# Optimization experiments

Measured on AMD Instinct MI355X. Metric: run time of the kernel, lower is better.

## Reference

```python
import jax, jax.numpy as jnp
import numpy as np

N, E = 50000, 500000
A, R, EB, EH, H, C, AH, SH, S, AV = 64, 20, 32, 64, 4, 32, 128, 64, 32, 32
EPS = 1e-8
MAX_DIST = 0.5   # nm, maximum_interaction_radius
SCALE = 1.0      # nm, scale_factor


def physnet_rbf(d):
    # PhysNet radial basis: exp(-beta * (exp(-d) - mu_k)^2), mu_k in [exp(-r_cut), 1]
    mu = jnp.linspace(np.exp(-MAX_DIST), 1.0, R).astype(jnp.float32)
    beta = jnp.float32((2.0 / R * (1.0 - np.exp(-MAX_DIST))) ** -2)
    return jnp.exp(-beta * (jnp.exp(-d)[:, None] - mu) ** 2)  # [E, R]


def _forward(h, x, v, idx_i, idx_j, W_edge_in, b_edge_in, W_edge_h, b_edge_h,
             W_edge_out, b_edge_out, W_att, b_att, W_x_mix, W_node1, b_node1,
             W_node2, b_node2, W_post1, b_post1, W_post2, b_post2,
             W_vel1, b_vel1, W_vel2, w_v_mix):
    n = h.shape[0]
    act = jax.nn.silu
    seg_sum = lambda t, idx: jax.ops.segment_sum(t, idx, num_segments=n)

    # geometry
    r_ij = x[idx_j] - x[idx_i]                       # [E,3]
    d_ij = jnp.sqrt(jnp.sum(r_ij * r_ij, -1) + EPS)  # [E]
    dir_ij = r_ij / (d_ij[:, None] + EPS)            # [E,3]

    # update_edge: gather, RBF filter, edge MLP
    h_cat = jnp.concatenate([h[idx_i], h[idx_j]], -1)                 # [E,2A]
    filtered = physnet_rbf(d_ij) * (h_cat @ W_edge_in + b_edge_in)    # [E,R]
    e_in = jnp.concatenate([h_cat, filtered, d_ij[:, None] / SCALE], -1)
    h_ij_edge = act(e_in @ W_edge_h + b_edge_h) @ W_edge_out + b_edge_out  # [E,EB]

    # semantic attention: CELU logits + segment softmax over receivers per head
    logits = jax.nn.celu(h_ij_edge @ W_att + b_att, alpha=2.0)        # [E,H]
    seg_max = jax.ops.segment_max(logits, idx_i, num_segments=n)      # [n,H]
    exp_l = jnp.exp(logits - seg_max[idx_i])
    denom = seg_sum(exp_l, idx_i)
    att = exp_l / (denom[idx_i] + EPS)                                # [E,H]
    h_ij_semantic = (att[:, :, None] * h_ij_edge[:, None, :]).reshape(-1, H * EB)

    # neighborhood aggregation (scatter-add)
    h_i_semantic = seg_sum(h_ij_semantic, idx_i)                      # [n,H*EB]

    # spatial attention
    mix = jnp.tanh(h_ij_semantic @ W_x_mix)                           # [E,C]
    combinations = dir_ij[:, None, :] * mix[:, :, None]               # [E,C,3]
    counts = jnp.maximum(seg_sum(jnp.ones((idx_i.shape[0],), h.dtype), idx_i), 1.0)
    comb_mean = seg_sum(combinations, idx_i) / counts[:, None, None]  # scatter-mean
    comb_norm2 = jnp.sum(comb_mean * comb_mean, -1)                   # [n,C]
    h_i_spatial = act(act(comb_norm2 @ W_post1 + b_post1) @ W_post2 + b_post2)

    # node update (residual)
    node_in = jnp.concatenate([h, h_i_semantic, h_i_spatial], -1)
    h_upd = h + act(act(node_in @ W_node1 + b_node1) @ W_node2 + b_node2)

    # velocity / coordinate update
    v_ij = jnp.einsum('ecx,c->ex', combinations, w_v_mix)             # [E,3]
    dv = seg_sum(v_ij, idx_i) / counts[:, None]                       # scatter-mean
    gate = 2.0 * jax.nn.sigmoid(act(h_upd @ W_vel1 + b_vel1) @ W_vel2)  # [n,1]
    v_upd = gate * v + dv
    x_upd = x + v_upd
    return h_upd, x_upd, v_upd


def _p(k, shape, scale=0.05):
    return jax.random.normal(k, shape, dtype=jnp.float32) * scale


def setup_inputs() -> dict:
    key = jax.random.key(0)
    ks = jax.random.split(key, 24)
    return {
        'h': jax.random.normal(ks[0], (N, A), dtype=jnp.float32),
        'x': jax.random.normal(ks[1], (N, 3), dtype=jnp.float32),
        'v': jax.random.normal(ks[2], (N, 3), dtype=jnp.float32),
        'idx_i': jax.random.randint(ks[3], (E,), 0, N),
        'idx_j': jax.random.randint(ks[4], (E,), 0, N),
        'W_edge_in': _p(ks[5], (2 * A, R)), 'b_edge_in': jnp.zeros((R,), jnp.float32),
        'W_edge_h': _p(ks[6], (2 * A + R + 1, EH)), 'b_edge_h': jnp.zeros((EH,), jnp.float32),
        'W_edge_out': _p(ks[7], (EH, EB)), 'b_edge_out': jnp.zeros((EB,), jnp.float32),
        'W_att': _p(ks[8], (EB, H)), 'b_att': jnp.zeros((H,), jnp.float32),
        'W_x_mix': _p(ks[9], (H * EB, C)),
        'W_node1': _p(ks[10], (A + H * EB + S, AH)), 'b_node1': jnp.zeros((AH,), jnp.float32),
        'W_node2': _p(ks[11], (AH, A)), 'b_node2': jnp.zeros((A,), jnp.float32),
        'W_post1': _p(ks[12], (C, SH)), 'b_post1': jnp.zeros((SH,), jnp.float32),
        'W_post2': _p(ks[13], (SH, S)), 'b_post2': jnp.zeros((S,), jnp.float32),
        'W_vel1': _p(ks[14], (A, AV)), 'b_vel1': jnp.zeros((AV,), jnp.float32),
        'W_vel2': _p(ks[15], (AV, 1)),
        'w_v_mix': _p(ks[16], (C,)),
    }


def reference(h, x, v, idx_i, idx_j, W_edge_in, b_edge_in, W_edge_h, b_edge_h,
              W_edge_out, b_edge_out, W_att, b_att, W_x_mix, W_node1, b_node1,
              W_node2, b_node2, W_post1, b_post1, W_post2, b_post2,
              W_vel1, b_vel1, W_vel2, w_v_mix):
    return _forward(h, x, v, idx_i, idx_j, W_edge_in, b_edge_in, W_edge_h, b_edge_h,
                    W_edge_out, b_edge_out, W_att, b_att, W_x_mix, W_node1, b_node1,
                    W_node2, b_node2, W_post1, b_post1, W_post2, b_post2,
                    W_vel1, b_vel1, W_vel2, w_v_mix)
```

## Files before the change

### kernel.cpp

```cpp
#include <hip/hip_runtime.h>
#include <math.h>

#define DA 64
#define NODEIN_DIM 224
#define EPSC 1e-8f

typedef short v8s __attribute__((ext_vector_type(8)));
typedef float v4f __attribute__((ext_vector_type(4)));
typedef unsigned short ushort_t;

__device__ __forceinline__ float siluf(float v) { return v / (1.0f + __expf(-v)); }

__device__ __forceinline__ void atomAddF(float* p, float v) {
#if defined(__HIP_DEVICE_COMPILE__)
  unsafeAtomicAdd(p, v);
#else
  atomicAdd(p, v);
#endif
}

__device__ __forceinline__ unsigned short f2bfu(float f) {
  union { float f; unsigned u; } v; v.f = f;
  unsigned r = v.u + 0x7fffu + ((v.u >> 16) & 1u);
  return (unsigned short)(r >> 16);
}
__device__ __forceinline__ short f2bfs(float f) { return (short)f2bfu(f); }
__device__ __forceinline__ float bf2f(ushort_t s) {
  union { unsigned u; float f; } v; v.u = ((unsigned)s) << 16; return v.f;
}

#define MU0 0.60653065971263342f
#define DMU ((1.0f - 0.60653065971263342f) / 19.0f)
#define BETA ((float)(1.0 / (0.039346934028736658 * 0.039346934028736658)))

__global__ __launch_bounds__(256) void cast_h(
    const float* __restrict__ hsrc, ushort_t* __restrict__ hb, int n4)
{
  const int i = blockIdx.x * blockDim.x + threadIdx.x;
  if (i < n4) {
    const float4 fv = ((const float4*)hsrc)[i];
    ushort4 o;
    o.x = f2bfu(fv.x); o.y = f2bfu(fv.y); o.z = f2bfu(fv.z); o.w = f2bfu(fv.w);
    ((ushort4*)hb)[i] = o;
  }
}

__global__ __launch_bounds__(256) void deg_count(
    const int* __restrict__ idx_i, int* __restrict__ deg, int E)
{
  const int stride = gridDim.x * blockDim.x;
  for (int e = blockIdx.x * blockDim.x + threadIdx.x; e < E; e += stride)
    atomicAdd(&deg[idx_i[e]], 1);
}

#define SCAN_B 64
#define SCAN_T (SCAN_B * 256)

__global__ __launch_bounds__(256) void deg_tsum(
    const int* __restrict__ deg, int* __restrict__ tsum, int N, int C)
{
  const int g = blockIdx.x * blockDim.x + threadIdx.x;
  const int lo = g * C;
  const int hi = (lo + C < N) ? (lo + C) : N;
  int s = 0;
  for (int i = lo; i < hi; ++i) s += deg[i];
  tsum[g] = s;
}

__global__ __launch_bounds__(256) void scan_tsum(int* __restrict__ tsum)
{
  __shared__ int ps[256];
  const int t = threadIdx.x;
  const int per = SCAN_T / 256;
  const int lo = t * per;
  int s = 0;
  for (int i = 0; i < per; ++i) s += tsum[lo + i];
  ps[t] = s;
  __syncthreads();
  if (t == 0) {
    int a = 0;
    for (int i = 0; i < 256; ++i) { const int v = ps[i]; ps[i] = a; a += v; }
  }
  __syncthreads();
  int acc = ps[t];
  for (int i = 0; i < per; ++i) {
    const int v = tsum[lo + i];
    tsum[lo + i] = acc;
    acc += v;
  }
}

__global__ __launch_bounds__(256) void write_csr(
    const int* __restrict__ deg, const int* __restrict__ tpre,
    int* __restrict__ rowstart, int* __restrict__ cursor,
    float* __restrict__ counts, int N, int C)
{
  const int g = blockIdx.x * blockDim.x + threadIdx.x;
  const int lo = g * C;
  const int hi = (lo + C < N) ? (lo + C) : N;
  int acc = tpre[g];
  for (int i = lo; i < hi; ++i) {
    const int d = deg[i];
    rowstart[i] = acc;
    cursor[i] = acc;
    counts[i] = (float)d;
    acc += d;
  }
  if (hi == N) rowstart[N] = acc;
}

__global__ __launch_bounds__(256) void bucket_edges(
    const int* __restrict__ idx_i, const int* __restrict__ idx_j,
    int* __restrict__ cursor, int* __restrict__ iperm,
    int* __restrict__ jperm, int E)
{
  const int stride = gridDim.x * blockDim.x;
  for (int e = blockIdx.x * blockDim.x + threadIdx.x; e < E; e += stride) {
    const int ii = idx_i[e];
    const int pos = atomicAdd(&cursor[ii], 1);
    iperm[pos] = ii;
    jperm[pos] = idx_j[e];
  }
}

#define THS 72
__global__ __launch_bounds__(256) void edge_f12(
    const ushort_t* __restrict__ h_bf, const float* __restrict__ x,
    const int* __restrict__ iperm, const int* __restrict__ jperm,
    const float* __restrict__ W_in, const float* __restrict__ b_in,
    const float* __restrict__ W_h, const float* __restrict__ b_h,
    const float* __restrict__ W_out, const float* __restrict__ b_out,
    const float* __restrict__ W_att, const float* __restrict__ b_att,
    float* __restrict__ dirb, ushort_t* __restrict__ heb,
    float* __restrict__ expl, float* __restrict__ denom, int E)
{
  __shared__ ushort_t sB1[8 * 512];
  __shared__ ushort_t sB2[20 * 512];
  __shared__ ushort_t tH[4][16 * THS];

  const int tid = threadIdx.x;
  for (int idx = tid; idx < 8 * 512; idx += 256) {
    const int j = idx & 7;
    const int ln = (idx >> 3) & 63;
    const int f = idx >> 9;
    const int k = (f >> 1) * 32 + (ln >> 4) * 8 + j;
    const int col = (f & 1) * 16 + (ln & 15);
    sB1[idx] = (col < 20) ? f2bfu(W_in[k * 20 + col]) : (ushort_t)0;
  }
  for (int idx = tid; idx < 20 * 512; idx += 256) {
    const int j = idx & 7;
    const int ln = (idx >> 3) & 63;
    const int f = idx >> 9;
    const int k = (f >> 2) * 32 + (ln >> 4) * 8 + j;
    const int col = (f & 3) * 16 + (ln & 15);
    sB2[idx] = (k < 149) ? f2bfu(W_h[k * 64 + col]) : (ushort_t)0;
  }
  __syncthreads();

  const int gtid = blockIdx.x * blockDim.x + tid;
  const int wid = gtid >> 6;
  const int lane = tid & 63;
  const int w = tid >> 6;
  const int nw = (gridDim.x * blockDim.x) >> 6;
  const int l15 = lane & 15;
  const int q = lane >> 4;

  const ushort_t* b1l = sB1 + lane * 8;
  const ushort_t* b2l = sB2 + lane * 8;

  v8s bfr3[2][2];
  #pragma unroll
  for (int kc = 0; kc < 2; ++kc)
    #pragma unroll
    for (int nt = 0; nt < 2; ++nt)
      #pragma unroll
      for (int j = 0; j < 8; ++j) {
        const int k = kc * 32 + q * 8 + j;
        const int col = nt * 16 + l15;
        bfr3[kc][nt][j] = f2bfs(W_out[k * 32 + col]);
      }

  float bin[2], mu[2];
  #pragma unroll
  for (int nt = 0; nt < 2; ++nt) {
    const int col = nt * 16 + l15;
    bin[nt] = (col < 20) ? b_in[col] : 0.0f;
    mu[nt] = MU0 + (float)col * DMU;
  }
  float bias2[4];
  #pragma unroll
  for (int nt = 0; nt < 4; ++nt) bias2[nt] = b_h[nt * 16 + l15];
  float bias3[2];
  #pragma unroll
  for (int nt = 0; nt < 2; ++nt) bias3[nt] = b_out[nt * 16 + l15];

  v8s battf;
  #pragma unroll
  for (int j = 0; j < 8; ++j)
    battf[j] = (l15 < 4) ? f2bfs(W_att[(q * 8 + j) * 4 + l15]) : (short)0;
  const float bav = (l15 < 4) ? b_att[l15] : 0.0f;

  const int ntiles = (E + 15) >> 4;

  int iiC = 0, jjC = 0;
  v8s afr[4];
  if (wid < ntiles) {
    const int row0 = wid * 16 + l15;
    const int rowL0 = (row0 < E) ? row0 : (E - 1);
    iiC = iperm[rowL0];
    jjC = jperm[rowL0];
    afr[0] = *(const v8s*)(h_bf + (size_t)iiC * 64 + q * 8);
    afr[1] = *(const v8s*)(h_bf + (size_t)iiC * 64 + 32 + q * 8);
    afr[2] = *(const v8s*)(h_bf + (size_t)jjC * 64 + q * 8);
    afr[3] = *(const v8s*)(h_bf + (size_t)jjC * 64 + 32 + q * 8);
  }

  for (int t = wid; t < ntiles; t += nw) {
    const int tn = t + nw;
    int iiN = 0, jjN = 0;
    v8s nfr[4];
    if (tn < ntiles) {
      const int rowN = tn * 16 + l15;
      const int rowLN = (rowN < E) ? rowN : (E - 1);
      iiN = iperm[rowLN];
      jjN = jperm[rowLN];
      nfr[0] = *(const v8s*)(h_bf + (size_t)iiN * 64 + q * 8);
      nfr[1] = *(const v8s*)(h_bf + (size_t)iiN * 64 + 32 + q * 8);
      nfr[2] = *(const v8s*)(h_bf + (size_t)jjN * 64 + q * 8);
      nfr[3] = *(const v8s*)(h_bf + (size_t)jjN * 64 + 32 + q * 8);
    }

    const int row = t * 16 + l15;
    float dval = 0.0f;
    if (lane < 16 && row < E) {
      const float rx = x[jjC * 3 + 0] - x[iiC * 3 + 0];
      const float ry = x[jjC * 3 + 1] - x[iiC * 3 + 1];
      const float rz = x[jjC * 3 + 2] - x[iiC * 3 + 2];
      const float d = sqrtf(rx * rx + ry * ry + rz * rz + EPSC);
      dval = d;
      const float inv = 1.0f / (d + EPSC);
      dirb[row * 3 + 0] = rx * inv;
      dirb[row * 3 + 1] = ry * inv;
      dirb[row * 3 + 2] = rz * inv;
    }

    v4f acc1[2];
    #pragma unroll
    for (int nt = 0; nt < 2; ++nt) {
      v4f a = {0.f, 0.f, 0.f, 0.f};
      #pragma unroll
      for (int kc = 0; kc < 4; ++kc) {
        const v8s bfrag = *(const v8s*)(b1l + (kc * 2 + nt) * 512);
        a = __builtin_amdgcn_mfma_f32_16x16x32_bf16(afr[kc], bfrag, a, 0, 0, 0);
      }
      acc1[nt] = a;
    }

    float dr[4], edr[4];
    #pragma unroll
    for (int r = 0; r < 4; ++r) {
      dr[r] = __shfl(dval, q * 4 + r);
      edr[r] = __expf(-dr[r]);
    }
    #pragma unroll
    for (int nt = 0; nt < 2; ++nt) {
      const int col = nt * 16 + l15;
      #pragma unroll
      for (int r = 0; r < 4; ++r) {
        ushort_t ov;
        if (col < 20) {
          const float tt = edr[r] - mu[nt];
          ov = f2bfu((acc1[nt][r] + bin[nt]) * __expf(-BETA * tt * tt));
        } else if (col == 20) {
          ov = f2bfu(dr[r]);
        } else {
          ov = 0;
        }
        tH[w][(q * 4 + r) * THS + col] = ov;
      }
    }
    __builtin_amdgcn_wave_barrier();

    const v8s afr4 = *(const v8s*)&tH[w][l15 * THS + q * 8];
    __builtin_amdgcn_wave_barrier();

    v4f acc2[4];
    #pragma unroll
    for (int nt = 0; nt < 4; ++nt) {
      v4f a = {0.f, 0.f, 0.f, 0.f};
      #pragma unroll
      for (int kc = 0; kc < 4; ++kc) {
        const v8s bfrag = *(const v8s*)(b2l + (kc * 4 + nt) * 512);
        a = __builtin_amdgcn_mfma_f32_16x16x32_bf16(afr[kc], bfrag, a, 0, 0, 0);
      }
      const v8s bfrag4 = *(const v8s*)(b2l + (4 * 4 + nt) * 512);
      a = __builtin_amdgcn_mfma_f32_16x16x32_bf16(afr4, bfrag4, a, 0, 0, 0);
      acc2[nt] = a;
    }

    #pragma unroll
    for (int nt = 0; nt < 4; ++nt) {
      #pragma unroll
      for (int r = 0; r < 4; ++r)
        tH[w][(q * 4 + r) * THS + nt * 16 + l15] =
            f2bfu(siluf(acc2[nt][r] + bias2[nt]));
    }
    __builtin_amdgcn_wave_barrier();

    v8s af3[2];
    af3[0] = *(const v8s*)&tH[w][l15 * THS + q * 8];
    af3[1] = *(const v8s*)&tH[w][l15 * THS + 32 + q * 8];

    v4f acc3[2];
    #pragma unroll
    for (int nt = 0; nt < 2; ++nt) {
      v4f a = {0.f, 0.f, 0.f, 0.f};
      #pragma unroll
      for (int kc = 0; kc < 2; ++kc)
        a = __builtin_amdgcn_mfma_f32_16x16x32_bf16(af3[kc], bfr3[kc][nt], a, 0, 0, 0);
      acc3[nt] = a;
    }
    __builtin_amdgcn_wave_barrier();

    const int rowb = t * 16 + q * 4;
    #pragma unroll
    for (int nt = 0; nt < 2; ++nt) {
      const int col = nt * 16 + l15;
      #pragma unroll
      for (int r = 0; r < 4; ++r) {
        const ushort_t hv = f2bfu(acc3[nt][r] + bias3[nt]);
        tH[w][(q * 4 + r) * THS + col] = hv;
        if (rowb + r < E) heb[(size_t)(rowb + r) * 32 + col] = hv;
      }
    }
    __builtin_amdgcn_wave_barrier();

    const v8s afA = *(const v8s*)&tH[w][l15 * THS + q * 8];
    v4f az = {0.f, 0.f, 0.f, 0.f};
    const v4f aacc = __builtin_amdgcn_mfma_f32_16x16x32_bf16(afA, battf, az, 0, 0, 0);

    int ii_r[4];
    #pragma unroll
    for (int r = 0; r < 4; ++r) ii_r[r] = __shfl(iiC, q * 4 + r);

    if (l15 < 4) {
      #pragma unroll
      for (int r = 0; r < 4; ++r) {
        if (rowb + r < E) {
          const float la = aacc[r] + bav;
          const float l = (la > 0.f) ? la : 2.0f * (__expf(0.5f * la) - 1.0f);
          const float ev = __expf(l);
          expl[(size_t)(rowb + r) * 4 + l15] = ev;
          atomAddF(&denom[ii_r[r] * 4 + l15], ev);
        }
      }
    }
    __builtin_amdgcn_wave_barrier();

    iiC = iiN; jjC = jjN;
    afr[0] = nfr[0]; afr[1] = nfr[1]; afr[2] = nfr[2]; afr[3] = nfr[3];
  }
}

__global__ __launch_bounds__(256) void mix_kernel(
    const ushort_t* __restrict__ heb, const int* __restrict__ iperm,
    const float* __restrict__ expl, const float* __restrict__ denom,
    const float* __restrict__ W_xmix, const float* __restrict__ w_vmix,
    ushort_t* __restrict__ mixE, float* __restrict__ pE, int E)
{
  const int tid = blockIdx.x * blockDim.x + threadIdx.x;
  const int wid = tid >> 6;
  const int lane = threadIdx.x & 63;
  const int nw = (gridDim.x * blockDim.x) >> 6;
  const int l15 = lane & 15;
  const int q = lane >> 4;

  v8s bfr[4][2];
  #pragma unroll
  for (int kc = 0; kc < 4; ++kc)
    #pragma unroll
    for (int nt = 0; nt < 2; ++nt)
      #pragma unroll
      for (int j = 0; j < 8; ++j) {
        const int k = kc * 32 + q * 8 + j;
        const int col = nt * 16 + l15;
        bfr[kc][nt][j] = f2bfs(W_xmix[k * 32 + col]);
      }
  float wv[2];
  wv[0] = w_vmix[l15];
  wv[1] = w_vmix[16 + l15];

  const int ntiles = (E + 15) >> 4;
  for (int t = wid; t < ntiles; t += nw) {
    const int row = t * 16 + l15;
    const int rowL = (row < E) ? row : (E - 1);
    const int ii = iperm[rowL];
    float att[4];
    #pragma unroll
    for (int hh = 0; hh < 4; ++hh)
      att[hh] = expl[(size_t)rowL * 4 + hh] / (denom[ii * 4 + hh] + EPSC);

    const v8s hech = *(const v8s*)(heb + (size_t)rowL * 32 + q * 8);
    float hef[8];
    #pragma unroll
    for (int j = 0; j < 8; ++j) hef[j] = bf2f((ushort_t)hech[j]);

    v8s afr[4];
    #pragma unroll
    for (int kc = 0; kc < 4; ++kc)
      #pragma unroll
      for (int j = 0; j < 8; ++j)
        afr[kc][j] = f2bfs(att[kc] * hef[j]);

    v4f acc[2];
    #pragma unroll
    for (int nt = 0; nt < 2; ++nt) {
      v4f a = {0.f, 0.f, 0.f, 0.f};
      #pragma unroll
      for (int kc = 0; kc < 4; ++kc)
        a = __builtin_amdgcn_mfma_f32_16x16x32_bf16(afr[kc], bfr[kc][nt], a, 0, 0, 0);
      acc[nt] = a;
    }

    const int rowb = t * 16 + q * 4;
    float pr[4];
    #pragma unroll
    for (int r = 0; r < 4; ++r) {
      const float m0 = tanhf(acc[0][r]);
      const float m1 = tanhf(acc[1][r]);
      if (rowb + r < E) {
        mixE[(size_t)(rowb + r) * 32 + l15] = f2bfu(m0);
        mixE[(size_t)(rowb + r) * 32 + 16 + l15] = f2bfu(m1);
      }
      pr[r] = m0 * wv[0] + m1 * wv[1];
    }
    #pragma unroll
    for (int r = 0; r < 4; ++r) {
      pr[r] += __shfl_xor(pr[r], 1);
      pr[r] += __shfl_xor(pr[r], 2);
      pr[r] += __shfl_xor(pr[r], 4);
      pr[r] += __shfl_xor(pr[r], 8);
      if (l15 == 0 && rowb + r < E) pE[rowb + r] = pr[r];
    }
  }
}

__global__ __launch_bounds__(256) void node_reduce(
    const int* __restrict__ rowstart,
    const ushort_t* __restrict__ heb, const ushort_t* __restrict__ mixE,
    const float* __restrict__ expl, const float* __restrict__ denom,
    const float* __restrict__ dirb, const float* __restrict__ pE,
    ushort_t* __restrict__ hsem, float* __restrict__ comb_sum,
    float* __restrict__ dv_sum, int N)
{
  const int tid = blockIdx.x * blockDim.x + threadIdx.x;
  const int wid = tid >> 6;
  const int lane = threadIdx.x & 63;
  const int nw = (gridDim.x * blockDim.x) >> 6;
  const int hh = lane >> 5;
  const int eb = lane & 31;

  for (int n = wid; n < N; n += nw) {
    const int s = rowstart[n];
    const int epd = rowstart[n + 1];
    float semA = 0.f, semB = 0.f;
    float cx = 0.f, cy = 0.f, cz = 0.f;
    float dvx = 0.f, dvy = 0.f, dvz = 0.f;
    int k = s;
    const int e4 = s + ((epd - s) & ~3);
    for (; k < e4; k += 4) {
      float he[4], ea[4], ec[4], dx[4], dy[4], dz[4], m[4], pe[4];
      #pragma unroll
      for (int u = 0; u < 4; ++u) {
        he[u] = bf2f(heb[(size_t)(k + u) * 32 + eb]);
        ea[u] = expl[(size_t)(k + u) * 4 + hh];
        ec[u] = expl[(size_t)(k + u) * 4 + 2 + hh];
        dx[u] = dirb[(k + u) * 3 + 0];
        dy[u] = dirb[(k + u) * 3 + 1];
        dz[u] = dirb[(k + u) * 3 + 2];
      }
      if (lane < 32) {
        #pragma unroll
        for (int u = 0; u < 4; ++u)
          m[u] = bf2f(mixE[(size_t)(k + u) * 32 + lane]);
      }
      if (lane == 0) {
        #pragma unroll
        for (int u = 0; u < 4; ++u) pe[u] = pE[k + u];
      }
      #pragma unroll
      for (int u = 0; u < 4; ++u) {
        semA += ea[u] * he[u];
        semB += ec[u] * he[u];
        if (lane < 32) {
          cx += dx[u] * m[u]; cy += dy[u] * m[u]; cz += dz[u] * m[u];
        }
        if (lane == 0) {
          dvx += dx[u] * pe[u]; dvy += dy[u] * pe[u]; dvz += dz[u] * pe[u];
        }
      }
    }
    for (; k < epd; ++k) {
      const float he = bf2f(heb[(size_t)k * 32 + eb]);
      const float ea = expl[(size_t)k * 4 + hh];
      const float ec = expl[(size_t)k * 4 + 2 + hh];
      semA += ea * he;
      semB += ec * he;
      const float dx = dirb[k * 3 + 0];
      const float dy = dirb[k * 3 + 1];
      const float dz = dirb[k * 3 + 2];
      if (lane < 32) {
        const float m = bf2f(mixE[(size_t)k * 32 + lane]);
        cx += dx * m; cy += dy * m; cz += dz * m;
      }
      if (lane == 0) {
        const float pe = pE[k];
        dvx += dx * pe; dvy += dy * pe; dvz += dz * pe;
      }
    }
    const float dA = denom[n * 4 + hh] + EPSC;
    const float dB = denom[n * 4 + 2 + hh] + EPSC;
    hsem[(size_t)n * 128 + lane] = f2bfu(semA / dA);
    hsem[(size_t)n * 128 + 64 + lane] = f2bfu(semB / dB);
    if (lane < 32) {
      comb_sum[(size_t)n * 96 + lane * 3 + 0] = cx;
      comb_sum[(size_t)n * 96 + lane * 3 + 1] = cy;
      comb_sum[(size_t)n * 96 + lane * 3 + 2] = cz;
    }
    if (lane == 0) {
      dv_sum[n * 3 + 0] = dvx;
      dv_sum[n * 3 + 1] = dvy;
      dv_sum[n * 3 + 2] = dvz;
    }
  }
}

#define W1S 232
__global__ __launch_bounds__(256) void node_c1_mfma(
    const ushort_t* __restrict__ h_bf, const ushort_t* __restrict__ hsem,
    const float* __restrict__ comb_sum, const float* __restrict__ counts,
    const float* __restrict__ W_post1, const float* __restrict__ b_post1,
    const float* __restrict__ W_post2, const float* __restrict__ b_post2,
    const float* __restrict__ W_node1, const float* __restrict__ b_node1,
    ushort_t* __restrict__ nh_out, int N)
{
  __shared__ ushort_t sW1t[128 * W1S];
  __shared__ ushort_t tp[4][16 * THS];

  const int tid = threadIdx.x;
  for (int idx = tid; idx < 224 * 128; idx += 256) {
    const int k = idx >> 7;
    const int c = idx & 127;
    sW1t[c * W1S + k] = f2bfu(W_node1[idx]);
  }
  __syncthreads();

  const int lane = tid & 63;
  const int w = tid >> 6;
  const int l15 = lane & 15;
  const int q = lane >> 4;

  v8s bp1[4];
  #pragma unroll
  for (int nt = 0; nt < 4; ++nt)
    #pragma unroll
    for (int j = 0; j < 8; ++j)
      bp1[nt][j] = f2bfs(W_post1[(q * 8 + j) * 64 + nt * 16 + l15]);
  v8s bp2[2][2];
  #pragma unroll
  for (int kc = 0; kc < 2; ++kc)
    #pragma unroll
    for (int nt = 0; nt < 2; ++nt)
      #pragma unroll
      for (int j = 0; j < 8; ++j)
        bp2[kc][nt][j] = f2bfs(W_post2[(kc * 32 + q * 8 + j) * 32 + nt * 16 + l15]);
  float bb1[4];
  #pragma unroll
  for (int nt = 0; nt < 4; ++nt) bb1[nt] = b_post1[nt * 16 + l15];
  float bb2[2];
  #pragma unroll
  for (int nt = 0; nt < 2; ++nt) bb2[nt] = b_post2[nt * 16 + l15];
  float b1[8];
  #pragma unroll
  for (int nt = 0; nt < 8; ++nt) b1[nt] = b_node1[nt * 16 + l15];

  const int gw = blockIdx.x * 4 + w;
  const int nwv = gridDim.x * 4;
  const int ntiles = (N + 15) >> 4;

  for (int t = gw; t < ntiles; t += nwv) {
    const int row = t * 16 + l15;
    const int rowL = (row < N) ? row : (N - 1);

    const float inv = 1.0f / fmaxf(counts[rowL], 1.0f);
    const float4* cs = (const float4*)(comb_sum + (size_t)rowL * 96 + q * 24);
    float cf[24];
    #pragma unroll
    for (int b = 0; b < 6; ++b) {
      const float4 cv = cs[b];
      cf[b * 4 + 0] = cv.x; cf[b * 4 + 1] = cv.y;
      cf[b * 4 + 2] = cv.z; cf[b * 4 + 3] = cv.w;
    }
    v8s a1;
    #pragma unroll
    for (int j = 0; j < 8; ++j) {
      const float vx = cf[j * 3 + 0] * inv;
      const float vy = cf[j * 3 + 1] * inv;
      const float vz = cf[j * 3 + 2] * inv;
      a1[j] = f2bfs(vx * vx + vy * vy + vz * vz);
    }

    v4f p1[4];
    #pragma unroll
    for (int nt = 0; nt < 4; ++nt) {
      v4f a = {0.f, 0.f, 0.f, 0.f};
      p1[nt] = __builtin_amdgcn_mfma_f32_16x16x32_bf16(a1, bp1[nt], a, 0, 0, 0);
    }
    #pragma unroll
    for (int nt = 0; nt < 4; ++nt)
      #pragma unroll
      for (int r = 0; r < 4; ++r)
        tp[w][(q * 4 + r) * THS + nt * 16 + l15] =
            f2bfu(siluf(p1[nt][r] + bb1[nt]));
    __builtin_amdgcn_wave_barrier();

    v8s a2[2];
    a2[0] = *(const v8s*)&tp[w][l15 * THS + q * 8];
    a2[1] = *(const v8s*)&tp[w][l15 * THS + 32 + q * 8];

    v4f p2[2];
    #pragma unroll
    for (int nt = 0; nt < 2; ++nt) {
      v4f a = {0.f, 0.f, 0.f, 0.f};
      #pragma unroll
      for (int kc = 0; kc < 2; ++kc)
        a = __builtin_amdgcn_mfma_f32_16x16x32_bf16(a2[kc], bp2[kc][nt], a, 0, 0, 0);
      p2[nt] = a;
    }
    __builtin_amdgcn_wave_barrier();
    #pragma unroll
    for (int nt = 0; nt < 2; ++nt)
      #pragma unroll
      for (int r = 0; r < 4; ++r)
        tp[w][(q * 4 + r) * THS + nt * 16 + l15] =
            f2bfu(siluf(p2[nt][r] + bb2[nt]));
    __builtin_amdgcn_wave_barrier();

    v8s af[7];
    af[0] = *(const v8s*)(h_bf + (size_t)rowL * 64 + q * 8);
    af[1] = *(const v8s*)(h_bf + (size_t)rowL * 64 + 32 + q * 8);
    #pragma unroll
    for (int kc = 0; kc < 4; ++kc)
      af[2 + kc] = *(const v8s*)(hsem + (size_t)rowL * 128 + kc * 32 + q * 8);
    af[6] = *(const v8s*)&tp[w][l15 * THS + q * 8];

    v4f acc[8];
    #pragma unroll
    for (int nt = 0; nt < 8; ++nt) acc[nt] = (v4f){0.f, 0.f, 0.f, 0.f};
    #pragma unroll
    for (int kc = 0; kc < 7; ++kc) {
      #pragma unroll
      for (int nt = 0; nt < 8; ++nt) {
        const v8s bfrag =
            *(const v8s*)&sW1t[(nt * 16 + l15) * W1S + kc * 32 + q * 8];
        acc[nt] = __builtin_amdgcn_mfma_f32_16x16x32_bf16(af[kc], bfrag, acc[nt], 0, 0, 0);
      }
    }

    const int rowb = t * 16 + q * 4;
    #pragma unroll
    for (int nt = 0; nt < 8; ++nt) {
      #pragma unroll
      for (int r = 0; r < 4; ++r)
        if (rowb + r < N)
          nh_out[(size_t)(rowb + r) * 128 + nt * 16 + l15] =
              f2bfu(siluf(acc[nt][r] + b1[nt]));
    }
  }
}

__global__ __launch_bounds__(256) void node_c2_mfma(
    const float* __restrict__ h, const float* __restrict__ x,
    const float* __restrict__ v, const ushort_t* __restrict__ nh,
    const float* __restrict__ dv_sum, const float* __restrict__ counts,
    const float* __restrict__ W_node2, const float* __restrict__ b_node2,
    const float* __restrict__ W_vel1, const float* __restrict__ b_vel1,
    const float* __restrict__ W_vel2,
    float* __restrict__ out, int N)
{
  __shared__ ushort_t sW2[16 * 64 * 8];
  __shared__ ushort_t sWv[4 * 64 * 8];
  __shared__ ushort_t tH[4][16 * THS];
  __shared__ float sg[4][16];

  const int tid = threadIdx.x;
  for (int idx = tid; idx < 16 * 64 * 8; idx += 256) {
    const int j = idx & 7;
    const int ln = (idx >> 3) & 63;
    const int f = idx >> 9;
    const int k = (f >> 2) * 32 + (ln >> 4) * 8 + j;
    const int col = (f & 3) * 16 + (ln & 15);
    sW2[idx] = f2bfu(W_node2[k * 64 + col]);
  }
  for (int idx = tid; idx < 4 * 64 * 8; idx += 256) {
    const int j = idx & 7;
    const int ln = (idx >> 3) & 63;
    const int f = idx >> 9;
    const int k = (f >> 1) * 32 + (ln >> 4) * 8 + j;
    const int col = (f & 1) * 16 + (ln & 15);
    sWv[idx] = f2bfu(W_vel1[k * 32 + col]);
  }
  __syncthreads();

  const int lane = tid & 63;
  const int w = tid >> 6;
  const int l15 = lane & 15;
  const int q = lane >> 4;

  const ushort_t* w2l = sW2 + lane * 8;
  const ushort_t* wvl = sWv + lane * 8;

  float b2[4];
  #pragma unroll
  for (int nt = 0; nt < 4; ++nt) b2[nt] = b_node2[nt * 16 + l15];
  float bv[2];
  #pragma unroll
  for (int nt = 0; nt < 2; ++nt) bv[nt] = b_vel1[nt * 16 + l15];
  float wv2[2];
  #pragma unroll
  for (int nt = 0; nt < 2; ++nt) wv2[nt] = W_vel2[nt * 16 + l15];

  const int gw = blockIdx.x * 4 + w;
  const int nwv = gridDim.x * 4;
  const int ntiles = (N + 15) >> 4;

  for (int t = gw; t < ntiles; t += nwv) {
    const int row = t * 16 + l15;
    const int rowL = (row < N) ? row : (N - 1);

    v8s af[4];
    #pragma unroll
    for (int kc = 0; kc < 4; ++kc)
      af[kc] = *(const v8s*)(nh + (size_t)rowL * 128 + kc * 32 + q * 8);

    v4f acc[4];
    #pragma unroll
    for (int nt = 0; nt < 4; ++nt) {
      v4f a = {0.f, 0.f, 0.f, 0.f};
      #pragma unroll
      for (int kc = 0; kc < 4; ++kc) {
        const v8s bfrag = *(const v8s*)(w2l + (kc * 4 + nt) * 512);
        a = __builtin_amdgcn_mfma_f32_16x16x32_bf16(af[kc], bfrag, a, 0, 0, 0);
      }
      acc[nt] = a;
    }

    const int rowb = t * 16 + q * 4;
    #pragma unroll
    for (int nt = 0; nt < 4; ++nt) {
      const int col = nt * 16 + l15;
      #pragma unroll
      for (int r = 0; r < 4; ++r) {
        const int n = rowb + r;
        if (n < N) {
          const float hu = h[(size_t)n * 64 + col] + siluf(acc[nt][r] + b2[nt]);
          out[(size_t)n * 64 + col] = hu;
          tH[w][(q * 4 + r) * THS + col] = f2bfu(hu);
        }
      }
    }
    __builtin_amdgcn_wave_barrier();

    v8s a2[2];
    a2[0] = *(const v8s*)&tH[w][l15 * THS + q * 8];
    a2[1] = *(const v8s*)&tH[w][l15 * THS + 32 + q * 8];
    v4f av[2];
    #pragma unroll
    for (int nt = 0; nt < 2; ++nt) {
      v4f a = {0.f, 0.f, 0.f, 0.f};
      #pragma unroll
      for (int kc = 0; kc < 2; ++kc) {
        const v8s bfrag = *(const v8s*)(wvl + (kc * 2 + nt) * 512);
        a = __builtin_amdgcn_mfma_f32_16x16x32_bf16(a2[kc], bfrag, a, 0, 0, 0);
      }
      av[nt] = a;
    }

    #pragma unroll
    for (int r = 0; r < 4; ++r) {
      float pr = siluf(av[0][r] + bv[0]) * wv2[0] +
                 siluf(av[1][r] + bv[1]) * wv2[1];
      pr += __shfl_xor(pr, 1);
      pr += __shfl_xor(pr, 2);
      pr += __shfl_xor(pr, 4);
      pr += __shfl_xor(pr, 8);
      if (l15 == 0) sg[w][q * 4 + r] = 2.0f / (1.0f + __expf(-pr));
    }
    __builtin_amdgcn_wave_barrier();

    if (lane < 48) {
      const int rr = lane / 3;
      const int c = lane % 3;
      const int n = t * 16 + rr;
      if (n < N) {
        const float gate = sg[w][rr];
        const float cnt = fmaxf(counts[n], 1.0f);
        const float dv = dv_sum[n * 3 + c] / cnt;
        const float vu = gate * v[n * 3 + c] + dv;
        out[(size_t)N * 64 + (size_t)n * 3 + c] = x[n * 3 + c] + vu;
        out[(size_t)N * 64 + (size_t)N * 3 + (size_t)n * 3 + c] = vu;
      }
    }
    __builtin_amdgcn_wave_barrier();
  }
}

extern "C" void kernel_launch(void* const* d_in, const int* in_sizes, int n_in,
                              void* d_out, int out_size, void* d_ws, size_t ws_size,
                              hipStream_t stream) {
  const float* h   = (const float*)d_in[0];
  const float* x   = (const float*)d_in[1];
  const float* v   = (const float*)d_in[2];
  const int* idx_i = (const int*)d_in[3];
  const int* idx_j = (const int*)d_in[4];
  const float* W_edge_in  = (const float*)d_in[5];
  const float* b_edge_in  = (const float*)d_in[6];
  const float* W_edge_h   = (const float*)d_in[7];
  const float* b_edge_h   = (const float*)d_in[8];
  const float* W_edge_out = (const float*)d_in[9];
  const float* b_edge_out = (const float*)d_in[10];
  const float* W_att      = (const float*)d_in[11];
  const float* b_att      = (const float*)d_in[12];
  const float* W_x_mix    = (const float*)d_in[13];
  const float* W_node1    = (const float*)d_in[14];
  const float* b_node1    = (const float*)d_in[15];
  const float* W_node2    = (const float*)d_in[16];
  const float* b_node2    = (const float*)d_in[17];
  const float* W_post1    = (const float*)d_in[18];
  const float* b_post1    = (const float*)d_in[19];
  const float* W_post2    = (const float*)d_in[20];
  const float* b_post2    = (const float*)d_in[21];
  const float* W_vel1     = (const float*)d_in[22];
  const float* b_vel1     = (const float*)d_in[23];
  const float* W_vel2     = (const float*)d_in[24];
  const float* w_v_mix    = (const float*)d_in[25];

  const int E = in_sizes[3];
  const int N = in_sizes[0] / DA;

  float* ws = (float*)d_ws;
  size_t off = 0;
  float* denom    = ws + off; off += (size_t)N * 4;
  int*   deg      = (int*)(ws + off); off += (size_t)N;
  const size_t zeroBytes = off * sizeof(float);
  float* counts   = ws + off; off += (size_t)N;
  int*   rowstart = (int*)(ws + off); off += (size_t)N + 4;
  int*   cursor   = (int*)(ws + off); off += (size_t)N;
  int*   tsum     = (int*)(ws + off); off += (size_t)SCAN_T;
  int*   iperm    = (int*)(ws + off); off += (size_t)E;
  int*   jperm    = (int*)(ws + off); off += (size_t)E;
  float* pE       = ws + off; off += (size_t)E;
  float* expl     = ws + off; off += (size_t)E * 4;
  float* dirb     = ws + off; off += (size_t)E * 3;
  float* hsemR    = ws + off; off += (size_t)N * 64;
  float* comb_sum = ws + off; off += (size_t)N * 96;
  float* dv_sum   = ws + off; off += (size_t)N * 4;
  float* hbfR     = ws + off; off += (size_t)N * 32;
  float* fltR     = ws + off; off += (size_t)E * 16;
  float* hebR     = ws + off; off += (size_t)E * 16;

  ushort_t* h_bf = (ushort_t*)hbfR;
  ushort_t* hsem = (ushort_t*)hsemR;
  ushort_t* heb  = (ushort_t*)hebR;
  ushort_t* mixE = (ushort_t*)fltR;
  ushort_t* nh   = (ushort_t*)fltR;

  hipMemsetAsync(d_ws, 0, zeroBytes, stream);

  {
    const int n4 = (N * 64) / 4;
    cast_h<<<(n4 + 255) / 256, 256, 0, stream>>>(h, h_bf, n4);
  }
  deg_count<<<512, 256, 0, stream>>>(idx_i, deg, E);
  {
    const int C = (N + SCAN_T - 1) / SCAN_T;
    deg_tsum<<<SCAN_B, 256, 0, stream>>>(deg, tsum, N, C);
    scan_tsum<<<1, 256, 0, stream>>>(tsum);
    write_csr<<<SCAN_B, 256, 0, stream>>>(deg, tsum, rowstart, cursor, counts, N, C);
  }
  bucket_edges<<<512, 256, 0, stream>>>(idx_i, idx_j, cursor, iperm, jperm, E);
  edge_f12<<<1024, 256, 0, stream>>>(h_bf, x, iperm, jperm,
                                     W_edge_in, b_edge_in, W_edge_h, b_edge_h,
                                     W_edge_out, b_edge_out, W_att, b_att,
                                     dirb, heb, expl, denom, E);
  mix_kernel<<<1024, 256, 0, stream>>>(heb, iperm, expl, denom, W_x_mix,
                                       w_v_mix, mixE, pE, E);
  node_reduce<<<2048, 256, 0, stream>>>(rowstart, heb, mixE, expl, denom,
                                        dirb, pE, hsem, comb_sum, dv_sum, N);
  node_c1_mfma<<<512, 256, 0, stream>>>(
      h_bf, hsem, comb_sum, counts, W_post1, b_post1, W_post2, b_post2,
      W_node1, b_node1, nh, N);
  node_c2_mfma<<<512, 256, 0, stream>>>(
      h, x, v, nh, dv_sum, counts, W_node2, b_node2, W_vel1, b_vel1, W_vel2,
      (float*)d_out, N);
}
```

Baseline: 410.5 us.

## Process two edge tiles per wave iteration with interleaved MFMA chains

The edge MLP kernel now handles two 16-edge tiles (A and B) per loop iteration, interleaving their MFMA chains and using separate LDS scratch buffers. This replaces the previous software prefetch of the next tile's gathered features. The goal is to expose independent MFMA work so the dependent accumulate chains and the epilogue latency overlap. The cost is higher register pressure and double the LDS scratch, which may lower occupancy, and the gather loads are no longer prefetched a tile ahead.

Result: no change. 404.6 us (-1.4%).

```diff
diff --git a/kernel.cpp b/kernel.cpp
--- a/kernel.cpp
+++ b/kernel.cpp
@@ -136,7 +136,8 @@
 {
   __shared__ ushort_t sB1[8 * 512];
   __shared__ ushort_t sB2[20 * 512];
-  __shared__ ushort_t tH[4][16 * THS];
+  __shared__ ushort_t tHA[4][16 * THS];
+  __shared__ ushort_t tHB[4][16 * THS];
 
   const int tid = threadIdx.x;
   for (int idx = tid; idx < 8 * 512; idx += 256) {
@@ -202,163 +203,207 @@
 
   const int ntiles = (E + 15) >> 4;
 
-  int iiC = 0, jjC = 0;
-  v8s afr[4];
-  if (wid < ntiles) {
-    const int row0 = wid * 16 + l15;
-    const int rowL0 = (row0 < E) ? row0 : (E - 1);
-    iiC = iperm[rowL0];
-    jjC = jperm[rowL0];
-    afr[0] = *(const v8s*)(h_bf + (size_t)iiC * 64 + q * 8);
-    afr[1] = *(const v8s*)(h_bf + (size_t)iiC * 64 + 32 + q * 8);
-    afr[2] = *(const v8s*)(h_bf + (size_t)jjC * 64 + q * 8);
-    afr[3] = *(const v8s*)(h_bf + (size_t)jjC * 64 + 32 + q * 8);
-  }
-
-  for (int t = wid; t < ntiles; t += nw) {
-    const int tn = t + nw;
-    int iiN = 0, jjN = 0;
-    v8s nfr[4];
-    if (tn < ntiles) {
-      const int rowN = tn * 16 + l15;
-      const int rowLN = (rowN < E) ? rowN : (E - 1);
-      iiN = iperm[rowLN];
-      jjN = jperm[rowLN];
-      nfr[0] = *(const v8s*)(h_bf + (size_t)iiN * 64 + q * 8);
-      nfr[1] = *(const v8s*)(h_bf + (size_t)iiN * 64 + 32 + q * 8);
-      nfr[2] = *(const v8s*)(h_bf + (size_t)jjN * 64 + q * 8);
-      nfr[3] = *(const v8s*)(h_bf + (size_t)jjN * 64 + 32 + q * 8);
-    }
-
-    const int row = t * 16 + l15;
-    float dval = 0.0f;
-    if (lane < 16 && row < E) {
-      const float rx = x[jjC * 3 + 0] - x[iiC * 3 + 0];
-      const float ry = x[jjC * 3 + 1] - x[iiC * 3 + 1];
-      const float rz = x[jjC * 3 + 2] - x[iiC * 3 + 2];
-      const float d = sqrtf(rx * rx + ry * ry + rz * rz + EPSC);
-      dval = d;
-      const float inv = 1.0f / (d + EPSC);
-      dirb[row * 3 + 0] = rx * inv;
-      dirb[row * 3 + 1] = ry * inv;
-      dirb[row * 3 + 2] = rz * inv;
-    }
-
-    v4f acc1[2];
+  for (int tA = wid; tA < ntiles; tA += 2 * nw) {
+    const int tBr = tA + nw;
+    const bool hasB = (tBr < ntiles);
+    const int tB = hasB ? tBr : tA;
+
+    const int rowA = tA * 16 + l15;
+    const int rowLA = (rowA < E) ? rowA : (E - 1);
+    const int iiA = iperm[rowLA];
+    const int jjA = jperm[rowLA];
+    const int rowB = tB * 16 + l15;
+    const int rowLB = (rowB < E) ? rowB : (E - 1);
+    const int iiB = iperm[rowLB];
+    const int jjB = jperm[rowLB];
+
+    v8s afrA[4], afrB[4];
+    afrA[0] = *(const v8s*)(h_bf + (size_t)iiA * 64 + q * 8);
+    afrA[1] = *(const v8s*)(h_bf + (size_t)iiA * 64 + 32 + q * 8);
+    afrA[2] = *(const v8s*)(h_bf + (size_t)jjA * 64 + q * 8);
+    afrA[3] = *(const v8s*)(h_bf + (size_t)jjA * 64 + 32 + q * 8);
+    afrB[0] = *(const v8s*)(h_bf + (size_t)iiB * 64 + q * 8);
+    afrB[1] = *(const v8s*)(h_bf + (size_t)iiB * 64 + 32 + q * 8);
+    afrB[2] = *(const v8s*)(h_bf + (size_t)jjB * 64 + q * 8);
+    afrB[3] = *(const v8s*)(h_bf + (size_t)jjB * 64 + 32 + q * 8);
+
+    float dvalA = 0.0f, dvalB = 0.0f;
+    if (lane < 16) {
+      if (rowA < E) {
+        const float rx = x[jjA * 3 + 0] - x[iiA * 3 + 0];
+        const float ry = x[jjA * 3 + 1] - x[iiA * 3 + 1];
+        const float rz = x[jjA * 3 + 2] - x[iiA * 3 + 2];
+        const float d = sqrtf(rx * rx + ry * ry + rz * rz + EPSC);
+        dvalA = d;
+        const float inv = 1.0f / (d + EPSC);
+        dirb[rowA * 3 + 0] = rx * inv;
+        dirb[rowA * 3 + 1] = ry * inv;
+        dirb[rowA * 3 + 2] = rz * inv;
+      }
+      if (hasB && rowB < E) {
+        const float rx = x[jjB * 3 + 0] - x[iiB * 3 + 0];
+        const float ry = x[jjB * 3 + 1] - x[iiB * 3 + 1];
+        const float rz = x[jjB * 3 + 2] - x[iiB * 3 + 2];
+        const float d = sqrtf(rx * rx + ry * ry + rz * rz + EPSC);
+        dvalB = d;
+        const float inv = 1.0f / (d + EPSC);
+        dirb[rowB * 3 + 0] = rx * inv;
+        dirb[rowB * 3 + 1] = ry * inv;
+        dirb[rowB * 3 + 2] = rz * inv;
+      }
+    }
+
+    v4f acc1A[2], acc1B[2];
     #pragma unroll
     for (int nt = 0; nt < 2; ++nt) {
       v4f a = {0.f, 0.f, 0.f, 0.f};
+      v4f b = {0.f, 0.f, 0.f, 0.f};
       #pragma unroll
       for (int kc = 0; kc < 4; ++kc) {
         const v8s bfrag = *(const v8s*)(b1l + (kc * 2 + nt) * 512);
-        a = __builtin_amdgcn_mfma_f32_16x16x32_bf16(afr[kc], bfrag, a, 0, 0, 0);
-      }
-      acc1[nt] = a;
-    }
-
-    float dr[4], edr[4];
+        a = __builtin_amdgcn_mfma_f32_16x16x32_bf16(afrA[kc], bfrag, a, 0, 0, 0);
+        b = __builtin_amdgcn_mfma_f32_16x16x32_bf16(afrB[kc], bfrag, b, 0, 0, 0);
+      }
+      acc1A[nt] = a;
+      acc1B[nt] = b;
+    }
+
+    float drA[4], edrA[4], drB[4], edrB[4];
     #pragma unroll
     for (int r = 0; r < 4; ++r) {
-      dr[r] = __shfl(dval, q * 4 + r);
-      edr[r] = __expf(-dr[r]);
+      drA[r] = __shfl(dvalA, q * 4 + r);
+      edrA[r] = __expf(-drA[r]);
+      drB[r] = __shfl(dvalB, q * 4 + r);
+      edrB[r] = __expf(-drB[r]);
     }
     #pragma unroll
     for (int nt = 0; nt < 2; ++nt) {
       const int col = nt * 16 + l15;
       #pragma unroll
       for (int r = 0; r < 4; ++r) {
-        ushort_t ov;
+        ushort_t ovA, ovB;
         if (col < 20) {
-          const float tt = edr[r] - mu[nt];
-          ov = f2bfu((acc1[nt][r] + bin[nt]) * __expf(-BETA * tt * tt));
+          const float ta = edrA[r] - mu[nt];
+          ovA = f2bfu((acc1A[nt][r] + bin[nt]) * __expf(-BETA * ta * ta));
+          const float tb = edrB[r] - mu[nt];
+          ovB = f2bfu((acc1B[nt][r] + bin[nt]) * __expf(-BETA * tb * tb));
         } else if (col == 20) {
-          ov = f2bfu(dr[r]);
+          ovA = f2bfu(drA[r]);
+          ovB = f2bfu(drB[r]);
         } else {
-          ov = 0;
+          ovA = 0; ovB = 0;
         }
-        tH[w][(q * 4 + r) * THS + col] = ov;
-      }
-    }
-    __builtin_amdgcn_wave_barrier();
-
-    const v8s afr4 = *(const v8s*)&tH[w][l15 * THS + q * 8];
-    __builtin_amdgcn_wave_barrier();
-
-    v4f acc2[4];
+        tHA[w][(q * 4 + r) * THS + col] = ovA;
+        tHB[w][(q * 4 + r) * THS + col] = ovB;
+      }
+    }
+    __builtin_amdgcn_wave_barrier();
+
+    const v8s afr4A = *(const v8s*)&tHA[w][l15 * THS + q * 8];
+    const v8s afr4B = *(const v8s*)&tHB[w][l15 * THS + q * 8];
+    __builtin_amdgcn_wave_barrier();
+
+    v4f acc2A[4], acc2B[4];
     #pragma unroll
     for (int nt = 0; nt < 4; ++nt) {
       v4f a = {0.f, 0.f, 0.f, 0.f};
+      v4f b = {0.f, 0.f, 0.f, 0.f};
       #pragma unroll
       for (int kc = 0; kc < 4; ++kc) {
         const v8s bfrag = *(const v8s*)(b2l + (kc * 4 + nt) * 512);
-        a = __builtin_amdgcn_mfma_f32_16x16x32_bf16(afr[kc], bfrag, a, 0, 0, 0);
+        a = __builtin_amdgcn_mfma_f32_16x16x32_bf16(afrA[kc], bfrag, a, 0, 0, 0);
+        b = __builtin_amdgcn_mfma_f32_16x16x32_bf16(afrB[kc], bfrag, b, 0, 0, 0);
       }
       const v8s bfrag4 = *(const v8s*)(b2l + (4 * 4 + nt) * 512);
-      a = __builtin_amdgcn_mfma_f32_16x16x32_bf16(afr4, bfrag4, a, 0, 0, 0);
-      acc2[nt] = a;
+      a = __builtin_amdgcn_mfma_f32_16x16x32_bf16(afr4A, bfrag4, a, 0, 0, 0);
+      b = __builtin_amdgcn_mfma_f32_16x16x32_bf16(afr4B, bfrag4, b, 0, 0, 0);
+      acc2A[nt] = a;
+      acc2B[nt] = b;
     }
 
     #pragma unroll
     for (int nt = 0; nt < 4; ++nt) {
       #pragma unroll
-      for (int r = 0; r < 4; ++r)
-        tH[w][(q * 4 + r) * THS + nt * 16 + l15] =
-            f2bfu(siluf(acc2[nt][r] + bias2[nt]));
-    }
-    __builtin_amdgcn_wave_barrier();
-
-    v8s af3[2];
-    af3[0] = *(const v8s*)&tH[w][l15 * THS + q * 8];
-    af3[1] = *(const v8s*)&tH[w][l15 * THS + 32 + q * 8];
-
-    v4f acc3[2];
+      for (int r = 0; r < 4; ++r) {
+        tHA[w][(q * 4 + r) * THS + nt * 16 + l15] =
+            f2bfu(siluf(acc2A[nt][r] + bias2[nt]));
+        tHB[w][(q * 4 + r) * THS + nt * 16 + l15] =
+            f2bfu(siluf(acc2B[nt][r] + bias2[nt]));
+      }
+    }
+    __builtin_amdgcn_wave_barrier();
+
+    v8s af3A[2], af3B[2];
+    af3A[0] = *(const v8s*)&tHA[w][l15 * THS + q * 8];
+    af3A[1] = *(const v8s*)&tHA[w][l15 * THS + 32 + q * 8];
+    af3B[0] = *(const v8s*)&tHB[w][l15 * THS + q * 8];
+    af3B[1] = *(const v8s*)&tHB[w][l15 * THS + 32 + q * 8];
+
+    v4f acc3A[2], acc3B[2];
     #pragma unroll
     for (int nt = 0; nt < 2; ++nt) {
       v4f a = {0.f, 0.f, 0.f, 0.f};
-      #pragma unroll
-      for (int kc = 0; kc < 2; ++kc)
-        a = __builtin_amdgcn_mfma_f32_16x16x32_bf16(af3[kc], bfr3[kc][nt], a, 0, 0, 0);
-      acc3[nt] = a;
-    }
-    __builtin_amdgcn_wave_barrier();
-
-    const int rowb = t * 16 + q * 4;
+      v4f b = {0.f, 0.f, 0.f, 0.f};
+      #pragma unroll
+      for (int kc = 0; kc < 2; ++kc) {
+        a = __builtin_amdgcn_mfma_f32_16x16x32_bf16(af3A[kc], bfr3[kc][nt], a, 0, 0, 0);
+        b = __builtin_amdgcn_mfma_f32_16x16x32_bf16(af3B[kc], bfr3[kc][nt], b, 0, 0, 0);
+      }
+      acc3A[nt] = a;
+      acc3B[nt] = b;
+    }
+    __builtin_amdgcn_wave_barrier();
+
+    const int rowbA = tA * 16 + q * 4;
+    const int rowbB = tB * 16 + q * 4;
     #pragma unroll
     for (int nt = 0; nt < 2; ++nt) {
       const int col = nt * 16 + l15;
       #pragma unroll
       for (int r = 0; r < 4; ++r) {
-        const ushort_t hv = f2bfu(acc3[nt][r] + bias3[nt]);
-        tH[w][(q * 4 + r) * THS + col] = hv;
-        if (rowb + r < E) heb[(size_t)(rowb + r) * 32 + col] = hv;
-      }
-    }
-    __builtin_amdgcn_wave_barrier();
-
-    const v8s afA = *(const v8s*)&tH[w][l15 * THS + q * 8];
+        const ushort_t hvA = f2bfu(acc3A[nt][r] + bias3[nt]);
+        tHA[w][(q * 4 + r) * THS + col] = hvA;
+        if (rowbA + r < E) heb[(size_t)(rowbA + r) * 32 + col] = hvA;
+        const ushort_t hvB = f2bfu(acc3B[nt][r] + bias3[nt]);
+        tHB[w][(q * 4 + r) * THS + col] = hvB;
+        if (hasB && rowbB + r < E) heb[(size_t)(rowbB + r) * 32 + col] = hvB;
+      }
+    }
+    __builtin_amdgcn_wave_barrier();
+
+    const v8s afAA = *(const v8s*)&tHA[w][l15 * THS + q * 8];
+    const v8s afAB = *(const v8s*)&tHB[w][l15 * THS + q * 8];
     v4f az = {0.f, 0.f, 0.f, 0.f};
-    const v4f aacc = __builtin_amdgcn_mfma_f32_16x16x32_bf16(afA, battf, az, 0, 0, 0);
-
-    int ii_r[4];
-    #pragma unroll
-    for (int r = 0; r < 4; ++r) ii_r[r] = __shfl(iiC, q * 4 + r);
+    const v4f aaccA = __builtin_amdgcn_mfma_f32_16x16x32_bf16(afAA, battf, az, 0, 0, 0);
+    const v4f aaccB = __builtin_amdgcn_mfma_f32_16x16x32_bf16(afAB, battf, az, 0, 0, 0);
+
+    int iiA_r[4], iiB_r[4];
+    #pragma unroll
+    for (int r = 0; r < 4; ++r) {
+      iiA_r[r] = __shfl(iiA, q * 4 + r);
+      iiB_r[r] = __shfl(iiB, q * 4 + r);
+    }
 
     if (l15 < 4) {
       #pragma unroll
       for (int r = 0; r < 4; ++r) {
-        if (rowb + r < E) {
-          const float la = aacc[r] + bav;
+        if (rowbA + r < E) {
+          const float la = aaccA[r] + bav;
           const float l = (la > 0.f) ? la : 2.0f * (__expf(0.5f * la) - 1.0f);
           const float ev = __expf(l);
-          expl[(size_t)(rowb + r) * 4 + l15] = ev;
-          atomAddF(&denom[ii_r[r] * 4 + l15], ev);
+          expl[(size_t)(rowbA + r) * 4 + l15] = ev;
+          atomAddF(&denom[iiA_r[r] * 4 + l15], ev);
         }
-      }
-    }
-    __builtin_amdgcn_wave_barrier();
-
-    iiC = iiN; jjC = jjN;
-    afr[0] = nfr[0]; afr[1] = nfr[1]; afr[2] = nfr[2]; afr[3] = nfr[3];
+        if (hasB && rowbB + r < E) {
+          const float la = aaccB[r] + bav;
+          const float l = (la > 0.f) ? la : 2.0f * (__expf(0.5f * la) - 1.0f);
+          const float ev = __expf(l);
+          expl[(size_t)(rowbB + r) * 4 + l15] = ev;
+          atomAddF(&denom[iiB_r[r] * 4 + l15], ev);
+        }
+      }
+    }
+    __builtin_amdgcn_wave_barrier();
   }
 }
 
```
